# Kernel optimization log

Hardware: AMD Instinct MI355X
Metric: run time of the kernel (lower is better)

The kernel has to match this reference:

```python
import jax, jax.numpy as jnp
import numpy as np

# LIF neuron constants (standard mem_update)
THRESH = 0.5
LENS = 0.5
DECAY = 0.25
EPS = 1e-5
NUM_HEADS = 8

@jax.custom_vjp
def act_fun(mem):
    return (mem > THRESH).astype(mem.dtype)

def _act_fwd(mem):
    return act_fun(mem), mem

def _act_bwd(mem, g):
    surrogate = (jnp.abs(mem - THRESH) < LENS).astype(g.dtype)
    return (g * surrogate,)

act_fun.defvjp(_act_fwd, _act_bwd)

def mem_update(x):
    # x: (T, ...) -> binary spikes (T, ...) via recurrent LIF dynamics
    def step(carry, xt):
        mem_old, spike = carry
        # spike is detached in the reset gate (torch .detach())
        mem = mem_old * DECAY * (1.0 - jax.lax.stop_gradient(spike)) + xt
        s = act_fun(mem)
        return (mem, s), s
    init = (jnp.zeros_like(x[0]), jnp.zeros_like(x[0]))
    _, out = jax.lax.scan(step, init, x)
    return out

def bn(x, gamma, beta, mean, var):
    # inference-mode BatchNorm1d over channel dim of (T,B,C,L)
    inv = gamma / jnp.sqrt(var + EPS)
    return x * inv[None, None, :, None] + (beta - mean * inv)[None, None, :, None]

def setup_inputs() -> dict:
    key = jax.random.key(0)
    ks = jax.random.split(key, 11)
    T, B, C, L = 4, 2, 384, 1024
    s = 1.0 / np.sqrt(C)
    return {
        "x": jax.random.normal(ks[0], (T, B, C, L), jnp.float32),
        "W_w": jax.random.normal(ks[1], (2 * C, C), jnp.float32) * s,
        "bn1_gamma": jax.random.uniform(ks[2], (2 * C,), jnp.float32, 0.5, 1.5),
        "bn1_beta": jax.random.normal(ks[3], (2 * C,), jnp.float32) * 0.1,
        "bn1_mean": jax.random.normal(ks[4], (2 * C,), jnp.float32) * 0.1,
        "bn1_var": jax.random.uniform(ks[5], (2 * C,), jnp.float32, 0.5, 1.5),
        "proj_w": jax.random.normal(ks[6], (C, C), jnp.float32) * s,
        "bn2_gamma": jax.random.uniform(ks[7], (C,), jnp.float32, 0.5, 1.5),
        "bn2_beta": jax.random.normal(ks[8], (C,), jnp.float32) * 0.1,
        "bn2_mean": jax.random.normal(ks[9], (C,), jnp.float32) * 0.1,
        "bn2_var": jax.random.uniform(ks[10], (C,), jnp.float32, 0.5, 1.5),
    }

def reference(x, W_w, bn1_gamma, bn1_beta, bn1_mean, bn1_var, proj_w, bn2_gamma, bn2_beta, bn2_mean, bn2_var):
    T, B, C, L = x.shape
    H = NUM_HEADS
    d = C // H
    x_feat = x
    xs = mem_update(x)                                   # binary spikes (T,B,C,L)
    y = jnp.einsum('oc,tbcl->tbol', W_w, xs)             # 1x1 conv C->2C
    y = bn(y, bn1_gamma, bn1_beta, bn1_mean, bn1_var)
    y = y.reshape(T, B, H, 2 * d, L)
    y1, y2 = y[:, :, :, :d, :], y[:, :, :, d:, :]
    xr = xs.reshape(T, B, H, d, L)
    attn = jnp.einsum('tbhdl,tbhdm->tbhlm', y1, xr)      # (L,L) per head
    attn = mem_update(attn)                              # binary spikes
    out = jnp.einsum('tbhdl,tbhlm->tbhdm', y2, attn)
    out = out.reshape(T, B, C, L)
    out = mem_update(out)
    out = jnp.einsum('oc,tbcl->tbol', proj_w, out)       # Wproj 1x1
    out = bn(out, bn2_gamma, bn2_beta, bn2_mean, bn2_var)
    return out + x_feat
```

## Files before the change

### kernel.cpp

```cpp
#include <hip/hip_runtime.h>

#define T_  4
#define B_  2
#define C_  384
#define L_  1024
#define H_  8
#define C2_ 768
#define S_  (B_*C_*L_)

typedef __attribute__((ext_vector_type(8))) short short8;
typedef __attribute__((ext_vector_type(4))) float floatx4;
typedef __attribute__((ext_vector_type(16))) float floatx16;

__device__ __forceinline__ unsigned bf16_rne(float v) {
    unsigned u = __float_as_uint(v);
    u += 0x7FFFu + ((u >> 16) & 1u);
    return u >> 16;
}
__device__ __forceinline__ float bf16_to_f(unsigned h) { return __uint_as_float(h << 16); }
__device__ __forceinline__ void split3(float v, unsigned& hi, unsigned& mi, unsigned& lo) {
    hi = bf16_rne(v);
    float r1 = v - bf16_to_f(hi);
    mi = bf16_rne(r1);
    float r2 = r1 - bf16_to_f(mi);
    lo = bf16_rne(r2);
}

__global__ __launch_bounds__(256) void split_w2(
    const float* __restrict__ Wa, int n4a,
    unsigned short* __restrict__ hia, unsigned short* __restrict__ mia,
    unsigned short* __restrict__ loa,
    const float* __restrict__ Wb, int n4b,
    unsigned short* __restrict__ hib, unsigned short* __restrict__ mib,
    unsigned short* __restrict__ lob) {
    int i = blockIdx.x * 256 + threadIdx.x;
    const float* W; unsigned short *hi, *mi, *lo;
    if (i < n4a) { W = Wa; hi = hia; mi = mia; lo = loa; }
    else {
        i -= n4a;
        if (i >= n4b) return;
        W = Wb; hi = hib; mi = mib; lo = lob;
    }
    float4 v = ((const float4*)W)[i];
    float vv[4] = {v.x, v.y, v.z, v.w};
    union { unsigned short us[4]; uint2 u2; } h, m, l;
#pragma unroll
    for (int e = 0; e < 4; e++) {
        unsigned hh, mm, ll; split3(vv[e], hh, mm, ll);
        h.us[e] = (unsigned short)hh; m.us[e] = (unsigned short)mm; l.us[e] = (unsigned short)ll;
    }
    ((uint2*)hi)[i] = h.u2; ((uint2*)mi)[i] = m.u2; ((uint2*)lo)[i] = l.u2;
}

__global__ __launch_bounds__(256) void scan_transpose(const float* __restrict__ src,
                                                      unsigned short* __restrict__ dstT) {
    __shared__ unsigned short tile[64][72];
    const int tid = threadIdx.x;
    const int l0 = blockIdx.x * 64, c0 = blockIdx.y * 64, b = blockIdx.z;
    const int row = tid >> 2, seg = tid & 3;
    float mem[16], sp[16];
#pragma unroll
    for (int e = 0; e < 16; e++) { mem[e] = 0.f; sp[e] = 0.f; }
    for (int t = 0; t < T_; t++) {
        const size_t base = ((size_t)((t*B_ + b)*C_ + c0 + row))*L_ + l0 + seg*16;
#pragma unroll
        for (int qq = 0; qq < 4; qq++) {
            float4 v = *(const float4*)(src + base + qq*4);
            float vv[4] = {v.x, v.y, v.z, v.w};
            unsigned bs[4];
#pragma unroll
            for (int s = 0; s < 4; s++) {
                int e = qq*4 + s;
                mem[e] = mem[e]*0.25f*(1.f - sp[e]) + vv[s];
                bool sb = mem[e] > 0.5f;
                sp[e] = sb ? 1.f : 0.f;
                bs[s] = sb ? 0x3F80u : 0u;
            }
            *(unsigned*)&tile[row][seg*16 + qq*4]     = bs[0] | (bs[1] << 16);
            *(unsigned*)&tile[row][seg*16 + qq*4 + 2] = bs[2] | (bs[3] << 16);
        }
        __syncthreads();
        {
            const int lr = tid >> 2, cs = tid & 3;
#pragma unroll
            for (int sub = 0; sub < 2; sub++) {
                unsigned wv[4];
#pragma unroll
                for (int p = 0; p < 4; p++) {
                    unsigned e0 = tile[cs*16 + sub*8 + p*2][lr];
                    unsigned e1 = tile[cs*16 + sub*8 + p*2 + 1][lr];
                    wv[p] = e0 | (e1 << 16);
                }
                uint4 o; o.x = wv[0]; o.y = wv[1]; o.z = wv[2]; o.w = wv[3];
                *(uint4*)(dstT + ((size_t)(t*B_ + b)*L_ + l0 + lr)*C_ + c0 + cs*16 + sub*8) = o;
            }
        }
        __syncthreads();
    }
}

__global__ __launch_bounds__(256) void gemm1_mfma(
    const unsigned short* __restrict__ whi, const unsigned short* __restrict__ wmi,
    const unsigned short* __restrict__ wlo, const unsigned short* __restrict__ xsT,
    const float* __restrict__ g, const float* __restrict__ be,
    const float* __restrict__ mn, const float* __restrict__ vr,
    unsigned short* __restrict__ y1hi, unsigned short* __restrict__ y1mi,
    unsigned short* __restrict__ y1lo,
    unsigned short* __restrict__ y2hi, unsigned short* __restrict__ y2mi,
    unsigned short* __restrict__ y2lo) {
    __shared__ unsigned short smem[14080];
    const int tid = threadIdx.x;
    const int flat = blockIdx.x;
    const int tb = flat & 7;
    const int ii = flat >> 3;
    const int mt = ii >> 4, lt = ii & 15;
    const int l0 = lt * 64;
    const int w = tid >> 6, lane = tid & 63;
    const int q = lane >> 4, n15 = lane & 15;
    const int mw = (w & 1) * 48, lw = (w >> 1) * 32;

    floatx4 acc[3][2];
#pragma unroll
    for (int i = 0; i < 3; i++)
#pragma unroll
        for (int j = 0; j < 2; j++) acc[i][j] = (floatx4){0.f,0.f,0.f,0.f};

    for (int ck = 0; ck < C_; ck += 32) {
#pragma unroll
        for (int p = 0; p < 3; p++) {
            const unsigned short* wp = p == 0 ? whi : p == 1 ? wmi : wlo;
            unsigned short* ap = smem + p*3840;
            for (int s = tid; s < 384; s += 256) {
                int r = s >> 2, c = s & 3;
                *(uint4*)&ap[r*40 + c*8] = *(const uint4*)(wp + (size_t)(mt*96 + r)*C_ + ck + c*8);
            }
        }
        {
            int r = tid >> 2, c = tid & 3;
            *(uint4*)&smem[11520 + r*40 + c*8] =
                *(const uint4*)(xsT + ((size_t)tb*L_ + l0 + r)*C_ + ck + c*8);
        }
        __syncthreads();
        short8 bb[2];
#pragma unroll
        for (int in = 0; in < 2; in++)
            bb[in] = *(short8*)&smem[11520 + (lw + in*16 + n15)*40 + q*8];
#pragma unroll
        for (int im = 0; im < 3; im++) {
            short8 ah = *(short8*)&smem[       (mw + im*16 + n15)*40 + q*8];
            short8 am = *(short8*)&smem[3840 + (mw + im*16 + n15)*40 + q*8];
            short8 al = *(short8*)&smem[7680 + (mw + im*16 + n15)*40 + q*8];
#pragma unroll
            for (int in = 0; in < 2; in++) {
                acc[im][in] = __builtin_amdgcn_mfma_f32_16x16x32_bf16(ah, bb[in], acc[im][in], 0,0,0);
                acc[im][in] = __builtin_amdgcn_mfma_f32_16x16x32_bf16(am, bb[in], acc[im][in], 0,0,0);
                acc[im][in] = __builtin_amdgcn_mfma_f32_16x16x32_bf16(al, bb[in], acc[im][in], 0,0,0);
            }
        }
        __syncthreads();
    }

#pragma unroll
    for (int im = 0; im < 3; im++)
#pragma unroll
        for (int r = 0; r < 4; r++) {
            int o = mt*96 + mw + im*16 + q*4 + r;
            float inv = g[o] / sqrtf(vr[o] + 1e-5f);
            float sh = be[o] - mn[o]*inv;
#pragma unroll
            for (int in = 0; in < 2; in++)
                acc[im][in][r] = acc[im][in][r]*inv + sh;
        }
    const bool isY1 = ((w & 1) == 0);
#pragma unroll
    for (int p = 0; p < 3; p++) {
        if (isY1) {
#pragma unroll
            for (int im = 0; im < 3; im++)
#pragma unroll
                for (int in = 0; in < 2; in++) {
                    union { unsigned short us[4]; uint2 u2; } pk;
#pragma unroll
                    for (int r = 0; r < 4; r++) {
                        unsigned hh = bf16_rne(acc[im][in][r]);
                        pk.us[r] = (unsigned short)hh;
                        acc[im][in][r] -= bf16_to_f(hh);
                    }
                    *(uint2*)&smem[(lw + in*16 + n15)*56 + im*16 + q*4] = pk.u2;
                }
        } else {
#pragma unroll
            for (int im = 0; im < 3; im++)
#pragma unroll
                for (int in = 0; in < 2; in++)
#pragma unroll
                    for (int r = 0; r < 4; r++) {
                        unsigned hh = bf16_rne(acc[im][in][r]);
                        smem[3584 + (im*16 + q*4 + r)*72 + lw + in*16 + n15] = (unsigned short)hh;
                        acc[im][in][r] -= bf16_to_f(hh);
                    }
        }
        __syncthreads();
        unsigned short* y1p = p == 0 ? y1hi : p == 1 ? y1mi : y1lo;
        unsigned short* y2p = p == 0 ? y2hi : p == 1 ? y2mi : y2lo;
        for (int s = tid; s < 384; s += 256) {
            int r1 = s / 6, c8 = s % 6;
            *(uint4*)(y1p + (((size_t)tb*H_ + mt)*L_ + l0 + r1)*48 + c8*8) =
                *(uint4*)&smem[r1*56 + c8*8];
        }
        for (int s = tid; s < 384; s += 256) {
            int cr = s >> 3, lq = s & 7;
            *(uint4*)(y2p + ((size_t)tb*C_ + mt*48 + cr)*L_ + l0 + lq*8) =
                *(uint4*)&smem[3584 + cr*72 + lq*8];
        }
        __syncthreads();
    }
}

__global__ __launch_bounds__(256) void attn_spike_mfma(
    const unsigned short* __restrict__ y1hi, const unsigned short* __restrict__ y1mi,
    const unsigned short* __restrict__ y1lo, const unsigned short* __restrict__ xsT,
    unsigned* __restrict__ bits) {
    __shared__ unsigned short A_hi[64][56], A_mi[64][56], A_lo[64][56], B_s[128][56];
    __shared__ unsigned bits_s[128][2];
    const int tid = threadIdx.x;
    const int flat = blockIdx.x;
    const int xcd = flat & 7;
    const int ii = flat >> 3;
    const int bh = xcd*2 + (ii >> 7);
    const int rr = ii & 127;
    const int b = bh >> 3, h = bh & 7;
    const int lbase = (rr >> 3) * 64;
    const int mbase = (rr & 7) * 128;
    const int w = tid >> 6, lane = tid & 63;
    const int l31 = lane & 31, half = lane >> 5;

    float mem[2][16];
#pragma unroll
    for (int il = 0; il < 2; il++)
#pragma unroll
        for (int r = 0; r < 16; r++) mem[il][r] = 0.f;

    for (int t = 0; t < T_; t++) {
        const int tb = t*B_ + b;
        const size_t yb = (((size_t)tb*H_ + h)*L_ + lbase)*48;
        const size_t xb = ((size_t)tb*L_ + mbase)*C_ + h*48;
        for (int s = tid; s < 384; s += 256) {
            int r = s / 6, c = s % 6;
            size_t ro = yb + (size_t)r*48 + c*8;
            *(uint4*)&A_hi[r][c*8] = *(const uint4*)(y1hi + ro);
            *(uint4*)&A_mi[r][c*8] = *(const uint4*)(y1mi + ro);
            *(uint4*)&A_lo[r][c*8] = *(const uint4*)(y1lo + ro);
        }
        for (int s = tid; s < 768; s += 256) {
            int r = s / 6, c = s % 6;
            *(uint4*)&B_s[r][c*8] = *(const uint4*)(xsT + xb + (size_t)r*C_ + c*8);
        }
        bits_s[tid >> 1][tid & 1] = 0u;
        __syncthreads();

        floatx16 acc[2];
#pragma unroll
        for (int il = 0; il < 2; il++)
#pragma unroll
            for (int r = 0; r < 16; r++) acc[il][r] = 0.f;

#pragma unroll
        for (int ks = 0; ks < 3; ks++) {
            const int kcol = ks*16 + half*8;
            short8 bb = *(short8*)&B_s[w*32 + l31][kcol];
#pragma unroll
            for (int il = 0; il < 2; il++) {
                short8 ah = *(short8*)&A_hi[il*32 + l31][kcol];
                short8 am = *(short8*)&A_mi[il*32 + l31][kcol];
                short8 al = *(short8*)&A_lo[il*32 + l31][kcol];
                acc[il] = __builtin_amdgcn_mfma_f32_32x32x16_bf16(ah, bb, acc[il], 0,0,0);
                acc[il] = __builtin_amdgcn_mfma_f32_32x32x16_bf16(am, bb, acc[il], 0,0,0);
                acc[il] = __builtin_amdgcn_mfma_f32_32x32x16_bf16(al, bb, acc[il], 0,0,0);
            }
        }

#pragma unroll
        for (int il = 0; il < 2; il++) {
            unsigned word = 0;
#pragma unroll
            for (int r = 0; r < 16; r++) {
                float m = (mem[il][r] > 0.5f ? 0.f : mem[il][r]*0.25f) + acc[il][r];
                mem[il][r] = m;
                int lloc = (r & 3) + 8*(r >> 2) + 4*half;
                word |= (m > 0.5f) ? (1u << lloc) : 0u;
            }
            atomicOr(&bits_s[w*32 + l31][il], word);
        }
        __syncthreads();
        {
            int m = tid >> 1, wd = tid & 1;
            bits[((size_t)(tb*H_ + h)*L_ + mbase + m)*32 + (lbase >> 5) + wd] = bits_s[m][wd];
        }
        __syncthreads();
    }
}

__global__ __launch_bounds__(256) void attn_out_mfma(
    const unsigned short* __restrict__ y2hi, const unsigned short* __restrict__ y2mi,
    const unsigned short* __restrict__ y2lo,
    const unsigned* __restrict__ bits, float* __restrict__ outpre) {
    __shared__ unsigned short A_hi[48][72], A_mi[48][72], A_lo[48][72];
    const int tid = threadIdx.x;
    const int flat = blockIdx.x;
    const int xcd = flat & 7;
    const int ii = flat >> 3;
    const int tbh = xcd*8 + (ii >> 3);
    const int mtile = ii & 7;
    const int t = tbh >> 4, b = (tbh >> 3) & 1, h = tbh & 7;
    const int tb = t*B_ + b;
    const int w = tid >> 6, lane = tid & 63;
    const int q = lane >> 4, n15 = lane & 15;
    const int mb = mtile*128 + w*32;

    floatx4 acc[3][2];
#pragma unroll
    for (int i = 0; i < 3; i++)
#pragma unroll
        for (int in = 0; in < 2; in++) acc[i][in] = (floatx4){0.f,0.f,0.f,0.f};

    const unsigned* brow0 = bits + ((size_t)(tb*H_ + h)*L_ + mb + n15)*32;
    const unsigned* brow1 = brow0 + 16*32;
    const size_t y2b = ((size_t)tb*C_ + h*48)*L_;

    for (int lt = 0; lt < L_; lt += 64) {
        for (int s = tid; s < 384; s += 256) {
            int r = s >> 3, c = s & 7;
            size_t ro = y2b + (size_t)r*L_ + lt + c*8;
            *(uint4*)&A_hi[r][c*8] = *(const uint4*)(y2hi + ro);
            *(uint4*)&A_mi[r][c*8] = *(const uint4*)(y2mi + ro);
            *(uint4*)&A_lo[r][c*8] = *(const uint4*)(y2lo + ro);
        }
        uint2 bw0 = *(const uint2*)(brow0 + (lt >> 5));
        uint2 bw1 = *(const uint2*)(brow1 + (lt >> 5));
        __syncthreads();
#pragma unroll
        for (int kc = 0; kc < 2; kc++) {
            unsigned word0 = kc ? bw0.y : bw0.x;
            unsigned word1 = kc ? bw1.y : bw1.x;
            unsigned byt0 = (word0 >> (q*8)) & 0xFFu;
            unsigned byt1 = (word1 >> (q*8)) & 0xFFu;
            union { unsigned u[4]; short8 v; } bu0, bu1;
#pragma unroll
            for (int p = 0; p < 4; p++) {
                bu0.u[p] = (((byt0 >> (2*p)) & 1u) ? 0x3F80u : 0u)
                         | (((byt0 >> (2*p+1)) & 1u) ? 0x3F800000u : 0u);
                bu1.u[p] = (((byt1 >> (2*p)) & 1u) ? 0x3F80u : 0u)
                         | (((byt1 >> (2*p+1)) & 1u) ? 0x3F800000u : 0u);
            }
            short8 bf0 = bu0.v, bf1 = bu1.v;
#pragma unroll
            for (int i = 0; i < 3; i++) {
                int ra = i*16 + n15;
                short8 ah = *(short8*)&A_hi[ra][kc*32 + q*8];
                short8 am = *(short8*)&A_mi[ra][kc*32 + q*8];
                short8 al = *(short8*)&A_lo[ra][kc*32 + q*8];
                acc[i][0] = __builtin_amdgcn_mfma_f32_16x16x32_bf16(ah, bf0, acc[i][0], 0,0,0);
                acc[i][0] = __builtin_amdgcn_mfma_f32_16x16x32_bf16(am, bf0, acc[i][0], 0,0,0);
                acc[i][0] = __builtin_amdgcn_mfma_f32_16x16x32_bf16(al, bf0, acc[i][0], 0,0,0);
                acc[i][1] = __builtin_amdgcn_mfma_f32_16x16x32_bf16(ah, bf1, acc[i][1], 0,0,0);
                acc[i][1] = __builtin_amdgcn_mfma_f32_16x16x32_bf16(am, bf1, acc[i][1], 0,0,0);
                acc[i][1] = __builtin_amdgcn_mfma_f32_16x16x32_bf16(al, bf1, acc[i][1], 0,0,0);
            }
        }
        __syncthreads();
    }
#pragma unroll
    for (int i = 0; i < 3; i++)
#pragma unroll
        for (int r = 0; r < 4; r++) {
            int d = i*16 + q*4 + r;
#pragma unroll
            for (int in = 0; in < 2; in++)
                outpre[((size_t)tb*C_ + h*48 + d)*L_ + mb + in*16 + n15] = acc[i][in][r];
        }
}

__global__ __launch_bounds__(256) void gemm2_mfma(
    const unsigned short* __restrict__ whi, const unsigned short* __restrict__ wmi,
    const unsigned short* __restrict__ wlo, const unsigned short* __restrict__ xT,
    const float* __restrict__ g, const float* __restrict__ be,
    const float* __restrict__ mn, const float* __restrict__ vr,
    const float* __restrict__ res, float* __restrict__ out) {
    __shared__ unsigned short A_hi[96][40], A_mi[96][40], A_lo[96][40];
    __shared__ unsigned short B_s[64][40];
    const int tid = threadIdx.x;
    const int tb = blockIdx.y;
    const int mt = blockIdx.x >> 4, lt = blockIdx.x & 15;
    const int l0 = lt * 64;
    const int w = tid >> 6, lane = tid & 63;
    const int q = lane >> 4, n15 = lane & 15;
    const int mw = (w & 1) * 48, lw = (w >> 1) * 32;

    floatx4 acc[3][2];
#pragma unroll
    for (int i = 0; i < 3; i++)
#pragma unroll
        for (int j = 0; j < 2; j++) acc[i][j] = (floatx4){0.f,0.f,0.f,0.f};

    for (int ck = 0; ck < C_; ck += 32) {
#pragma unroll
        for (int p = 0; p < 3; p++) {
            const unsigned short* wp = p == 0 ? whi : p == 1 ? wmi : wlo;
            unsigned short (*ap)[40] = p == 0 ? A_hi : p == 1 ? A_mi : A_lo;
            for (int s = tid; s < 384; s += 256) {
                int r = s >> 2, c = s & 3;
                *(uint4*)&ap[r][c*8] = *(const uint4*)(wp + (size_t)(mt*96 + r)*C_ + ck + c*8);
            }
        }
        {
            int r = tid >> 2, c4 = tid & 3;
            *(uint4*)&B_s[r][c4*8] = *(const uint4*)(xT + ((size_t)tb*L_ + l0 + r)*C_ + ck + c4*8);
        }
        __syncthreads();
        short8 bb[2];
#pragma unroll
        for (int in = 0; in < 2; in++)
            bb[in] = *(short8*)&B_s[lw + in*16 + n15][q*8];
#pragma unroll
        for (int im = 0; im < 3; im++) {
            short8 ah = *(short8*)&A_hi[mw + im*16 + n15][q*8];
            short8 am = *(short8*)&A_mi[mw + im*16 + n15][q*8];
            short8 al = *(short8*)&A_lo[mw + im*16 + n15][q*8];
#pragma unroll
            for (int in = 0; in < 2; in++) {
                acc[im][in] = __builtin_amdgcn_mfma_f32_16x16x32_bf16(ah, bb[in], acc[im][in], 0,0,0);
                acc[im][in] = __builtin_amdgcn_mfma_f32_16x16x32_bf16(am, bb[in], acc[im][in], 0,0,0);
                acc[im][in] = __builtin_amdgcn_mfma_f32_16x16x32_bf16(al, bb[in], acc[im][in], 0,0,0);
            }
        }
        __syncthreads();
    }
#pragma unroll
    for (int im = 0; im < 3; im++)
#pragma unroll
        for (int r = 0; r < 4; r++) {
            int o = mt*96 + mw + im*16 + q*4 + r;
            float inv = g[o] / sqrtf(vr[o] + 1e-5f);
            float sh = be[o] - mn[o]*inv;
#pragma unroll
            for (int in = 0; in < 2; in++) {
                int l = l0 + lw + in*16 + n15;
                size_t idx = ((size_t)tb*C_ + o)*L_ + l;
                out[idx] = acc[im][in][r]*inv + sh + res[idx];
            }
        }
}

extern "C" void kernel_launch(void* const* d_in, const int* in_sizes, int n_in,
                              void* d_out, int out_size, void* d_ws, size_t ws_size,
                              hipStream_t stream) {
    const float* x   = (const float*)d_in[0];
    const float* W_w = (const float*)d_in[1];
    const float* g1  = (const float*)d_in[2];
    const float* b1  = (const float*)d_in[3];
    const float* m1  = (const float*)d_in[4];
    const float* v1  = (const float*)d_in[5];
    const float* pw  = (const float*)d_in[6];
    const float* g2  = (const float*)d_in[7];
    const float* b2  = (const float*)d_in[8];
    const float* m2  = (const float*)d_in[9];
    const float* v2  = (const float*)d_in[10];

    float* ws = (float*)d_ws;
    unsigned short* xsT  = (unsigned short*)ws;
    unsigned short* y1hi = (unsigned short*)(ws + 1572864);
    unsigned short* y1mi = (unsigned short*)(ws + 3145728);
    unsigned short* y1lo = (unsigned short*)(ws + 4718592);
    unsigned short* y2hi = (unsigned short*)(ws + 6291456);
    unsigned short* y2mi = (unsigned short*)(ws + 7864320);
    unsigned short* y2lo = (unsigned short*)(ws + 9437184);
    unsigned*       bits = (unsigned*)(ws + 11010048);
    unsigned short* wspl[3]  = {(unsigned short*)(ws + 13107200),
                                (unsigned short*)(ws + 13254656),
                                (unsigned short*)(ws + 13402112)};
    unsigned short* pwspl[3] = {(unsigned short*)(ws + 13549568),
                                (unsigned short*)(ws + 13623296),
                                (unsigned short*)(ws + 13697024)};
    float*          outpre = (float*)(ws + 1572864);
    unsigned short* outsT  = (unsigned short*)(ws + 4718592);
    float* out = (float*)d_out;

    split_w2<<<dim3(432), 256, 0, stream>>>(W_w, C2_*C_/4, wspl[0], wspl[1], wspl[2],
                                            pw,  C_*C_/4, pwspl[0], pwspl[1], pwspl[2]);
    scan_transpose<<<dim3(16, 6, B_), 256, 0, stream>>>(x, xsT);
    gemm1_mfma<<<dim3(1024), 256, 0, stream>>>(wspl[0], wspl[1], wspl[2], xsT,
                                               g1, b1, m1, v1,
                                               y1hi, y1mi, y1lo, y2hi, y2mi, y2lo);
    attn_spike_mfma<<<dim3(2048), 256, 0, stream>>>(y1hi, y1mi, y1lo, xsT, bits);
    attn_out_mfma<<<dim3(512), 256, 0, stream>>>(y2hi, y2mi, y2lo, bits, outpre);
    scan_transpose<<<dim3(16, 6, B_), 256, 0, stream>>>(outpre, outsT);
    gemm2_mfma<<<dim3(64, 8), 256, 0, stream>>>(pwspl[0], pwspl[1], pwspl[2], outsT,
                                                g2, b2, m2, v2, x, out);
}
```

Before: 222.2 us.

## Fuse all stages into one persistent kernel with software grid barriers

Replaces the seven separate launches (weight split, two scan-transposes, two GEMMs, two attention kernels) with a single persistent kernel of 512 blocks. The stages are separated by an atomic-counter grid barrier, with each block looping over the jobs of each phase. The goal is to remove per-launch overhead and the tail gaps between kernels. In exchange the grid is fixed at 512 blocks, so the scan phases leave most blocks idle and the split and scan work share an epoch. Correctness depends on all blocks being co-resident, and the barrier has a spin timeout that could break silently.

```diff
diff --git a/kernel.cpp b/kernel.cpp
--- a/kernel.cpp
+++ b/kernel.cpp
@@ -6,7 +6,7 @@
 #define L_  1024
 #define H_  8
 #define C2_ 768
-#define S_  (B_*C_*L_)
+#define NB_ 512
 
 typedef __attribute__((ext_vector_type(8))) short short8;
 typedef __attribute__((ext_vector_type(4))) float floatx4;
@@ -26,37 +26,43 @@
     lo = bf16_rne(r2);
 }
 
-__global__ __launch_bounds__(256) void split_w2(
-    const float* __restrict__ Wa, int n4a,
-    unsigned short* __restrict__ hia, unsigned short* __restrict__ mia,
-    unsigned short* __restrict__ loa,
-    const float* __restrict__ Wb, int n4b,
-    unsigned short* __restrict__ hib, unsigned short* __restrict__ mib,
-    unsigned short* __restrict__ lob) {
-    int i = blockIdx.x * 256 + threadIdx.x;
-    const float* W; unsigned short *hi, *mi, *lo;
-    if (i < n4a) { W = Wa; hi = hia; mi = mia; lo = loa; }
-    else {
-        i -= n4a;
-        if (i >= n4b) return;
-        W = Wb; hi = hib; mi = mib; lo = lob;
-    }
-    float4 v = ((const float4*)W)[i];
-    float vv[4] = {v.x, v.y, v.z, v.w};
-    union { unsigned short us[4]; uint2 u2; } h, m, l;
-#pragma unroll
-    for (int e = 0; e < 4; e++) {
-        unsigned hh, mm, ll; split3(vv[e], hh, mm, ll);
-        h.us[e] = (unsigned short)hh; m.us[e] = (unsigned short)mm; l.us[e] = (unsigned short)ll;
-    }
-    ((uint2*)hi)[i] = h.u2; ((uint2*)mi)[i] = m.u2; ((uint2*)lo)[i] = l.u2;
-}
-
-__global__ __launch_bounds__(256) void scan_transpose(const float* __restrict__ src,
-                                                      unsigned short* __restrict__ dstT) {
-    __shared__ unsigned short tile[64][72];
-    const int tid = threadIdx.x;
-    const int l0 = blockIdx.x * 64, c0 = blockIdx.y * 64, b = blockIdx.z;
+struct Params {
+    const float *x, *W_w, *g1, *b1, *m1, *v1, *pw, *g2, *b2, *m2, *v2;
+    unsigned short *xsT, *y1hi, *y1mi, *y1lo, *y2hi, *y2mi, *y2lo;
+    unsigned *bits;
+    unsigned short *whi, *wmi, *wlo, *pwhi, *pwmi, *pwlo;
+    float *outpre; unsigned short *outsT;
+    float *out;
+    unsigned *bar;
+};
+
+__device__ __forceinline__ void grid_barrier(unsigned* bar, int tid) {
+    __syncthreads();
+    if (tid == 0) {
+        __threadfence();
+        unsigned a = __hip_atomic_fetch_add(&bar[0], 1u, __ATOMIC_ACQ_REL,
+                                            __HIP_MEMORY_SCOPE_AGENT);
+        unsigned target = (a >> 9) + 1u;
+        if ((a + 1u) % NB_ == 0u)
+            __hip_atomic_fetch_add(&bar[1], 1u, __ATOMIC_ACQ_REL,
+                                   __HIP_MEMORY_SCOPE_AGENT);
+        unsigned spin = 0;
+        while (__hip_atomic_load(&bar[1], __ATOMIC_ACQUIRE,
+                                 __HIP_MEMORY_SCOPE_AGENT) < target) {
+            if (++spin > 500000u) break;
+            __builtin_amdgcn_s_sleep(8);
+        }
+        __threadfence();
+    }
+    __syncthreads();
+}
+
+__device__ void scan_body(const float* __restrict__ src, unsigned short* __restrict__ dstT,
+                          int job, int tid, unsigned char* smraw) {
+    unsigned short (*tile)[72] = (unsigned short (*)[72])smraw;
+    const int l0 = (job & 15) * 64;
+    const int c0 = ((job >> 4) % 6) * 64;
+    const int b  = job / 96;
     const int row = tid >> 2, seg = tid & 3;
     float mem[16], sp[16];
 #pragma unroll
@@ -99,18 +105,8 @@
     }
 }
 
-__global__ __launch_bounds__(256) void gemm1_mfma(
-    const unsigned short* __restrict__ whi, const unsigned short* __restrict__ wmi,
-    const unsigned short* __restrict__ wlo, const unsigned short* __restrict__ xsT,
-    const float* __restrict__ g, const float* __restrict__ be,
-    const float* __restrict__ mn, const float* __restrict__ vr,
-    unsigned short* __restrict__ y1hi, unsigned short* __restrict__ y1mi,
-    unsigned short* __restrict__ y1lo,
-    unsigned short* __restrict__ y2hi, unsigned short* __restrict__ y2mi,
-    unsigned short* __restrict__ y2lo) {
-    __shared__ unsigned short smem[14080];
-    const int tid = threadIdx.x;
-    const int flat = blockIdx.x;
+__device__ void gemm1_body(const Params& p, int flat, int tid, unsigned char* smraw) {
+    unsigned short* smem = (unsigned short*)smraw;
     const int tb = flat & 7;
     const int ii = flat >> 3;
     const int mt = ii >> 4, lt = ii & 15;
@@ -127,9 +123,9 @@
 
     for (int ck = 0; ck < C_; ck += 32) {
 #pragma unroll
-        for (int p = 0; p < 3; p++) {
-            const unsigned short* wp = p == 0 ? whi : p == 1 ? wmi : wlo;
-            unsigned short* ap = smem + p*3840;
+        for (int pp = 0; pp < 3; pp++) {
+            const unsigned short* wp = pp == 0 ? p.whi : pp == 1 ? p.wmi : p.wlo;
+            unsigned short* ap = smem + pp*3840;
             for (int s = tid; s < 384; s += 256) {
                 int r = s >> 2, c = s & 3;
                 *(uint4*)&ap[r*40 + c*8] = *(const uint4*)(wp + (size_t)(mt*96 + r)*C_ + ck + c*8);
@@ -138,7 +134,7 @@
         {
             int r = tid >> 2, c = tid & 3;
             *(uint4*)&smem[11520 + r*40 + c*8] =
-                *(const uint4*)(xsT + ((size_t)tb*L_ + l0 + r)*C_ + ck + c*8);
+                *(const uint4*)(p.xsT + ((size_t)tb*L_ + l0 + r)*C_ + ck + c*8);
         }
         __syncthreads();
         short8 bb[2];
@@ -165,15 +161,15 @@
 #pragma unroll
         for (int r = 0; r < 4; r++) {
             int o = mt*96 + mw + im*16 + q*4 + r;
-            float inv = g[o] / sqrtf(vr[o] + 1e-5f);
-            float sh = be[o] - mn[o]*inv;
+            float inv = p.g1[o] / sqrtf(p.v1[o] + 1e-5f);
+            float sh = p.b1[o] - p.m1[o]*inv;
 #pragma unroll
             for (int in = 0; in < 2; in++)
                 acc[im][in][r] = acc[im][in][r]*inv + sh;
         }
     const bool isY1 = ((w & 1) == 0);
 #pragma unroll
-    for (int p = 0; p < 3; p++) {
+    for (int pp = 0; pp < 3; pp++) {
         if (isY1) {
 #pragma unroll
             for (int im = 0; im < 3; im++)
@@ -201,8 +197,8 @@
                     }
         }
         __syncthreads();
-        unsigned short* y1p = p == 0 ? y1hi : p == 1 ? y1mi : y1lo;
-        unsigned short* y2p = p == 0 ? y2hi : p == 1 ? y2mi : y2lo;
+        unsigned short* y1p = pp == 0 ? p.y1hi : pp == 1 ? p.y1mi : p.y1lo;
+        unsigned short* y2p = pp == 0 ? p.y2hi : pp == 1 ? p.y2mi : p.y2lo;
         for (int s = tid; s < 384; s += 256) {
             int r1 = s / 6, c8 = s % 6;
             *(uint4*)(y1p + (((size_t)tb*H_ + mt)*L_ + l0 + r1)*48 + c8*8) =
@@ -217,18 +213,15 @@
     }
 }
 
-__global__ __launch_bounds__(256) void attn_spike_mfma(
-    const unsigned short* __restrict__ y1hi, const unsigned short* __restrict__ y1mi,
-    const unsigned short* __restrict__ y1lo, const unsigned short* __restrict__ xsT,
-    unsigned* __restrict__ bits) {
-    __shared__ unsigned short A_hi[64][56], A_mi[64][56], A_lo[64][56], B_s[128][56];
-    __shared__ unsigned bits_s[128][2];
-    const int tid = threadIdx.x;
-    const int flat = blockIdx.x;
-    const int xcd = flat & 7;
-    const int ii = flat >> 3;
-    const int bh = xcd*2 + (ii >> 7);
-    const int rr = ii & 127;
+__device__ void attn_spike_body(const Params& p, int job, int tid, unsigned char* smraw) {
+    unsigned short (*A_hi)[56] = (unsigned short (*)[56])(smraw);
+    unsigned short (*A_mi)[56] = (unsigned short (*)[56])(smraw + 7168);
+    unsigned short (*A_lo)[56] = (unsigned short (*)[56])(smraw + 14336);
+    unsigned short (*B_s)[56]  = (unsigned short (*)[56])(smraw + 21504);
+    unsigned (*bits_s)[2]      = (unsigned (*)[2])(smraw + 35840);
+
+    const int bh = job >> 7;
+    const int rr = job & 127;
     const int b = bh >> 3, h = bh & 7;
     const int lbase = (rr >> 3) * 64;
     const int mbase = (rr & 7) * 128;
@@ -248,13 +241,13 @@
         for (int s = tid; s < 384; s += 256) {
             int r = s / 6, c = s % 6;
             size_t ro = yb + (size_t)r*48 + c*8;
-            *(uint4*)&A_hi[r][c*8] = *(const uint4*)(y1hi + ro);
-            *(uint4*)&A_mi[r][c*8] = *(const uint4*)(y1mi + ro);
-            *(uint4*)&A_lo[r][c*8] = *(const uint4*)(y1lo + ro);
+            *(uint4*)&A_hi[r][c*8] = *(const uint4*)(p.y1hi + ro);
+            *(uint4*)&A_mi[r][c*8] = *(const uint4*)(p.y1mi + ro);
+            *(uint4*)&A_lo[r][c*8] = *(const uint4*)(p.y1lo + ro);
         }
         for (int s = tid; s < 768; s += 256) {
             int r = s / 6, c = s % 6;
-            *(uint4*)&B_s[r][c*8] = *(const uint4*)(xsT + xb + (size_t)r*C_ + c*8);
+            *(uint4*)&B_s[r][c*8] = *(const uint4*)(p.xsT + xb + (size_t)r*C_ + c*8);
         }
         bits_s[tid >> 1][tid & 1] = 0u;
         __syncthreads();
@@ -295,23 +288,19 @@
         __syncthreads();
         {
             int m = tid >> 1, wd = tid & 1;
-            bits[((size_t)(tb*H_ + h)*L_ + mbase + m)*32 + (lbase >> 5) + wd] = bits_s[m][wd];
-        }
-        __syncthreads();
-    }
-}
-
-__global__ __launch_bounds__(256) void attn_out_mfma(
-    const unsigned short* __restrict__ y2hi, const unsigned short* __restrict__ y2mi,
-    const unsigned short* __restrict__ y2lo,
-    const unsigned* __restrict__ bits, float* __restrict__ outpre) {
-    __shared__ unsigned short A_hi[48][72], A_mi[48][72], A_lo[48][72];
-    const int tid = threadIdx.x;
-    const int flat = blockIdx.x;
-    const int xcd = flat & 7;
-    const int ii = flat >> 3;
-    const int tbh = xcd*8 + (ii >> 3);
-    const int mtile = ii & 7;
+            p.bits[((size_t)(tb*H_ + h)*L_ + mbase + m)*32 + (lbase >> 5) + wd] = bits_s[m][wd];
+        }
+        __syncthreads();
+    }
+}
+
+__device__ void attn_out_body(const Params& p, int job, int tid, unsigned char* smraw) {
+    unsigned short (*A_hi)[72] = (unsigned short (*)[72])(smraw);
+    unsigned short (*A_mi)[72] = (unsigned short (*)[72])(smraw + 6912);
+    unsigned short (*A_lo)[72] = (unsigned short (*)[72])(smraw + 13824);
+
+    const int tbh = job >> 3;
+    const int mtile = job & 7;
     const int t = tbh >> 4, b = (tbh >> 3) & 1, h = tbh & 7;
     const int tb = t*B_ + b;
     const int w = tid >> 6, lane = tid & 63;
@@ -324,7 +313,7 @@
 #pragma unroll
         for (int in = 0; in < 2; in++) acc[i][in] = (floatx4){0.f,0.f,0.f,0.f};
 
-    const unsigned* brow0 = bits + ((size_t)(tb*H_ + h)*L_ + mb + n15)*32;
+    const unsigned* brow0 = p.bits + ((size_t)(tb*H_ + h)*L_ + mb + n15)*32;
     const unsigned* brow1 = brow0 + 16*32;
     const size_t y2b = ((size_t)tb*C_ + h*48)*L_;
 
@@ -332,9 +321,9 @@
         for (int s = tid; s < 384; s += 256) {
             int r = s >> 3, c = s & 7;
             size_t ro = y2b + (size_t)r*L_ + lt + c*8;
-            *(uint4*)&A_hi[r][c*8] = *(const uint4*)(y2hi + ro);
-            *(uint4*)&A_mi[r][c*8] = *(const uint4*)(y2mi + ro);
-            *(uint4*)&A_lo[r][c*8] = *(const uint4*)(y2lo + ro);
+            *(uint4*)&A_hi[r][c*8] = *(const uint4*)(p.y2hi + ro);
+            *(uint4*)&A_mi[r][c*8] = *(const uint4*)(p.y2mi + ro);
+            *(uint4*)&A_lo[r][c*8] = *(const uint4*)(p.y2lo + ro);
         }
         uint2 bw0 = *(const uint2*)(brow0 + (lt >> 5));
         uint2 bw1 = *(const uint2*)(brow1 + (lt >> 5));
@@ -347,11 +336,11 @@
             unsigned byt1 = (word1 >> (q*8)) & 0xFFu;
             union { unsigned u[4]; short8 v; } bu0, bu1;
 #pragma unroll
-            for (int p = 0; p < 4; p++) {
-                bu0.u[p] = (((byt0 >> (2*p)) & 1u) ? 0x3F80u : 0u)
-                         | (((byt0 >> (2*p+1)) & 1u) ? 0x3F800000u : 0u);
-                bu1.u[p] = (((byt1 >> (2*p)) & 1u) ? 0x3F80u : 0u)
-                         | (((byt1 >> (2*p+1)) & 1u) ? 0x3F800000u : 0u);
+            for (int pp = 0; pp < 4; pp++) {
+                bu0.u[pp] = (((byt0 >> (2*pp)) & 1u) ? 0x3F80u : 0u)
+                          | (((byt0 >> (2*pp+1)) & 1u) ? 0x3F800000u : 0u);
+                bu1.u[pp] = (((byt1 >> (2*pp)) & 1u) ? 0x3F80u : 0u)
+                          | (((byt1 >> (2*pp+1)) & 1u) ? 0x3F800000u : 0u);
             }
             short8 bf0 = bu0.v, bf1 = bu1.v;
 #pragma unroll
@@ -377,21 +366,19 @@
             int d = i*16 + q*4 + r;
 #pragma unroll
             for (int in = 0; in < 2; in++)
-                outpre[((size_t)tb*C_ + h*48 + d)*L_ + mb + in*16 + n15] = acc[i][in][r];
-        }
-}
-
-__global__ __launch_bounds__(256) void gemm2_mfma(
-    const unsigned short* __restrict__ whi, const unsigned short* __restrict__ wmi,
-    const unsigned short* __restrict__ wlo, const unsigned short* __restrict__ xT,
-    const float* __restrict__ g, const float* __restrict__ be,
-    const float* __restrict__ mn, const float* __restrict__ vr,
-    const float* __restrict__ res, float* __restrict__ out) {
-    __shared__ unsigned short A_hi[96][40], A_mi[96][40], A_lo[96][40];
-    __shared__ unsigned short B_s[64][40];
-    const int tid = threadIdx.x;
-    const int tb = blockIdx.y;
-    const int mt = blockIdx.x >> 4, lt = blockIdx.x & 15;
+                p.outpre[((size_t)tb*C_ + h*48 + d)*L_ + mb + in*16 + n15] = acc[i][in][r];
+        }
+}
+
+__device__ void gemm2_body(const Params& p, int job, int tid, unsigned char* smraw) {
+    unsigned short (*A_hi)[40] = (unsigned short (*)[40])(smraw);
+    unsigned short (*A_mi)[40] = (unsigned short (*)[40])(smraw + 7680);
+    unsigned short (*A_lo)[40] = (unsigned short (*)[40])(smraw + 15360);
+    unsigned short (*B_s)[40]  = (unsigned short (*)[40])(smraw + 23040);
+
+    const int tb = job & 7;
+    const int xx = job >> 3;
+    const int mt = xx >> 4, lt = xx & 15;
     const int l0 = lt * 64;
     const int w = tid >> 6, lane = tid & 63;
     const int q = lane >> 4, n15 = lane & 15;
@@ -405,9 +392,9 @@
 
     for (int ck = 0; ck < C_; ck += 32) {
 #pragma unroll
-        for (int p = 0; p < 3; p++) {
-            const unsigned short* wp = p == 0 ? whi : p == 1 ? wmi : wlo;
-            unsigned short (*ap)[40] = p == 0 ? A_hi : p == 1 ? A_mi : A_lo;
+        for (int pp = 0; pp < 3; pp++) {
+            const unsigned short* wp = pp == 0 ? p.pwhi : pp == 1 ? p.pwmi : p.pwlo;
+            unsigned short (*ap)[40] = pp == 0 ? A_hi : pp == 1 ? A_mi : A_lo;
             for (int s = tid; s < 384; s += 256) {
                 int r = s >> 2, c = s & 3;
                 *(uint4*)&ap[r][c*8] = *(const uint4*)(wp + (size_t)(mt*96 + r)*C_ + ck + c*8);
@@ -415,7 +402,7 @@
         }
         {
             int r = tid >> 2, c4 = tid & 3;
-            *(uint4*)&B_s[r][c4*8] = *(const uint4*)(xT + ((size_t)tb*L_ + l0 + r)*C_ + ck + c4*8);
+            *(uint4*)&B_s[r][c4*8] = *(const uint4*)(p.outsT + ((size_t)tb*L_ + l0 + r)*C_ + ck + c4*8);
         }
         __syncthreads();
         short8 bb[2];
@@ -441,60 +428,93 @@
 #pragma unroll
         for (int r = 0; r < 4; r++) {
             int o = mt*96 + mw + im*16 + q*4 + r;
-            float inv = g[o] / sqrtf(vr[o] + 1e-5f);
-            float sh = be[o] - mn[o]*inv;
+            float inv = p.g2[o] / sqrtf(p.v2[o] + 1e-5f);
+            float sh = p.b2[o] - p.m2[o]*inv;
 #pragma unroll
             for (int in = 0; in < 2; in++) {
                 int l = l0 + lw + in*16 + n15;
                 size_t idx = ((size_t)tb*C_ + o)*L_ + l;
-                out[idx] = acc[im][in][r]*inv + sh + res[idx];
-            }
-        }
+                p.out[idx] = acc[im][in][r]*inv + sh + p.x[idx];
+            }
+        }
+}
+
+__global__ __launch_bounds__(256, 2) void mega(Params p) {
+    __shared__ __align__(16) unsigned char smraw[36864];
+    const int bid = blockIdx.x, tid = threadIdx.x;
+
+    {
+        const int n4a = C2_*C_/4, n4b = C_*C_/4;
+        int i = bid*256 + tid;
+        if (i < n4a + n4b) {
+            const float* W; unsigned short *hi, *mi, *lo;
+            if (i < n4a) { W = p.W_w; hi = p.whi; mi = p.wmi; lo = p.wlo; }
+            else { i -= n4a; W = p.pw; hi = p.pwhi; mi = p.pwmi; lo = p.pwlo; }
+            float4 v = ((const float4*)W)[i];
+            float vv[4] = {v.x, v.y, v.z, v.w};
+            union { unsigned short us[4]; uint2 u2; } h, m, l;
+#pragma unroll
+            for (int e = 0; e < 4; e++) {
+                unsigned hh, mm, ll; split3(vv[e], hh, mm, ll);
+                h.us[e] = (unsigned short)hh; m.us[e] = (unsigned short)mm; l.us[e] = (unsigned short)ll;
+            }
+            ((uint2*)hi)[i] = h.u2; ((uint2*)mi)[i] = m.u2; ((uint2*)lo)[i] = l.u2;
+        }
+    }
+    if (bid < 192) scan_body(p.x, p.xsT, bid, tid, smraw);
+    grid_barrier(p.bar, tid);
+
+    for (int r = 0; r < 2; r++) gemm1_body(p, bid*2 + r, tid, smraw);
+    grid_barrier(p.bar, tid);
+
+    for (int r = 0; r < 4; r++) attn_spike_body(p, bid*4 + r, tid, smraw);
+    grid_barrier(p.bar, tid);
+
+    attn_out_body(p, bid, tid, smraw);
+    grid_barrier(p.bar, tid);
+
+    if (bid < 192) scan_body(p.outpre, p.outsT, bid, tid, smraw);
+    grid_barrier(p.bar, tid);
+
+    gemm2_body(p, bid, tid, smraw);
 }
 
 extern "C" void kernel_launch(void* const* d_in, const int* in_sizes, int n_in,
                               void* d_out, int out_size, void* d_ws, size_t ws_size,
                               hipStream_t stream) {
-    const float* x   = (const float*)d_in[0];
-    const float* W_w = (const float*)d_in[1];
-    const float* g1  = (const float*)d_in[2];
-    const float* b1  = (const float*)d_in[3];
-    const float* m1  = (const float*)d_in[4];
-    const float* v1  = (const float*)d_in[5];
-    const float* pw  = (const float*)d_in[6];
-    const float* g2  = (const float*)d_in[7];
-    const float* b2  = (const float*)d_in[8];
-    const float* m2  = (const float*)d_in[9];
-    const float* v2  = (const float*)d_in[10];
-
     float* ws = (float*)d_ws;
-    unsigned short* xsT  = (unsigned short*)ws;
-    unsigned short* y1hi = (unsigned short*)(ws + 1572864);
-    unsigned short* y1mi = (unsigned short*)(ws + 3145728);
-    unsigned short* y1lo = (unsigned short*)(ws + 4718592);
-    unsigned short* y2hi = (unsigned short*)(ws + 6291456);
-    unsigned short* y2mi = (unsigned short*)(ws + 7864320);
-    unsigned short* y2lo = (unsigned short*)(ws + 9437184);
-    unsigned*       bits = (unsigned*)(ws + 11010048);
-    unsigned short* wspl[3]  = {(unsigned short*)(ws + 13107200),
-                                (unsigned short*)(ws + 13254656),
-                                (unsigned short*)(ws + 13402112)};
-    unsigned short* pwspl[3] = {(unsigned short*)(ws + 13549568),
-                                (unsigned short*)(ws + 13623296),
-                                (unsigned short*)(ws + 13697024)};
-    float*          outpre = (float*)(ws + 1572864);
-    unsigned short* outsT  = (unsigned short*)(ws + 4718592);
-    float* out = (float*)d_out;
-
-    split_w2<<<dim3(432), 256, 0, stream>>>(W_w, C2_*C_/4, wspl[0], wspl[1], wspl[2],
-                                            pw,  C_*C_/4, pwspl[0], pwspl[1], pwspl[2]);
-    scan_transpose<<<dim3(16, 6, B_), 256, 0, stream>>>(x, xsT);
-    gemm1_mfma<<<dim3(1024), 256, 0, stream>>>(wspl[0], wspl[1], wspl[2], xsT,
-                                               g1, b1, m1, v1,
-                                               y1hi, y1mi, y1lo, y2hi, y2mi, y2lo);
-    attn_spike_mfma<<<dim3(2048), 256, 0, stream>>>(y1hi, y1mi, y1lo, xsT, bits);
-    attn_out_mfma<<<dim3(512), 256, 0, stream>>>(y2hi, y2mi, y2lo, bits, outpre);
-    scan_transpose<<<dim3(16, 6, B_), 256, 0, stream>>>(outpre, outsT);
-    gemm2_mfma<<<dim3(64, 8), 256, 0, stream>>>(pwspl[0], pwspl[1], pwspl[2], outsT,
-                                                g2, b2, m2, v2, x, out);
-}
+    Params p;
+    p.x   = (const float*)d_in[0];
+    p.W_w = (const float*)d_in[1];
+    p.g1  = (const float*)d_in[2];
+    p.b1  = (const float*)d_in[3];
+    p.m1  = (const float*)d_in[4];
+    p.v1  = (const float*)d_in[5];
+    p.pw  = (const float*)d_in[6];
+    p.g2  = (const float*)d_in[7];
+    p.b2  = (const float*)d_in[8];
+    p.m2  = (const float*)d_in[9];
+    p.v2  = (const float*)d_in[10];
+
+    p.xsT  = (unsigned short*)ws;
+    p.y1hi = (unsigned short*)(ws + 1572864);
+    p.y1mi = (unsigned short*)(ws + 3145728);
+    p.y1lo = (unsigned short*)(ws + 4718592);
+    p.y2hi = (unsigned short*)(ws + 6291456);
+    p.y2mi = (unsigned short*)(ws + 7864320);
+    p.y2lo = (unsigned short*)(ws + 9437184);
+    p.bits = (unsigned*)(ws + 11010048);
+    p.whi  = (unsigned short*)(ws + 13107200);
+    p.wmi  = (unsigned short*)(ws + 13254656);
+    p.wlo  = (unsigned short*)(ws + 13402112);
+    p.pwhi = (unsigned short*)(ws + 13549568);
+    p.pwmi = (unsigned short*)(ws + 13623296);
+    p.pwlo = (unsigned short*)(ws + 13697024);
+    p.outpre = (float*)(ws + 1572864);
+    p.outsT  = (unsigned short*)(ws + 4718592);
+    p.out = (float*)d_out;
+    p.bar = (unsigned*)(ws + 13900800);
+
+    hipMemsetAsync(p.bar, 0, 2*sizeof(unsigned), stream);
+    mega<<<dim3(NB_), dim3(256), 0, stream>>>(p);
+}
```

New measurement: 680.7 us. 3.06x slower.
